# Kernel optimization log

Measured on AMD Instinct MI355X. Metric: run time of the kernel, lower is better.

## Reference

```python
import jax, jax.numpy as jnp
import numpy as np

GROUP = 128  # quantization group size along the input dimension


def dequant(q, scales, zeros):
    # q: [out, in] int4 codes stored as int32 in [0,16)
    # scales, zeros: [out, in//GROUP] per-group affine params
    out_dim, in_dim = q.shape
    g = in_dim // GROUP
    w = (q.astype(jnp.float32).reshape(out_dim, g, GROUP) - zeros[:, :, None]) * scales[:, :, None]
    return w.reshape(out_dim, in_dim)


def setup_inputs() -> dict:
    key = jax.random.key(0)
    ks = jax.random.split(key, 10)
    H, I = 4096, 11008
    B, S = 64, 1
    inp = {
        "x": jax.random.normal(ks[0], (B, S, H), dtype=jnp.float32),
        "gate_qweight": jax.random.randint(ks[1], (I, H), 0, 16, dtype=jnp.int32),
        "gate_scales": jax.random.uniform(ks[2], (I, H // GROUP), dtype=jnp.float32) * 0.02,
        "gate_zeros": jax.random.uniform(ks[3], (I, H // GROUP), dtype=jnp.float32) * 16.0,
        "up_qweight": jax.random.randint(ks[4], (I, H), 0, 16, dtype=jnp.int32),
        "up_scales": jax.random.uniform(ks[5], (I, H // GROUP), dtype=jnp.float32) * 0.02,
        "up_zeros": jax.random.uniform(ks[6], (I, H // GROUP), dtype=jnp.float32) * 16.0,
        "down_qweight": jax.random.randint(ks[7], (H, I), 0, 16, dtype=jnp.int32),
        "down_scales": jax.random.uniform(ks[8], (H, I // GROUP), dtype=jnp.float32) * 0.02,
        "down_zeros": jax.random.uniform(ks[9], (H, I // GROUP), dtype=jnp.float32) * 16.0,
    }
    return inp


def reference(x, gate_qweight, gate_scales, gate_zeros,
              up_qweight, up_scales, up_zeros,
              down_qweight, down_scales, down_zeros):
    Wg = dequant(gate_qweight, gate_scales, gate_zeros)   # [I, H]
    Wu = dequant(up_qweight, up_scales, up_zeros)         # [I, H]
    Wd = dequant(down_qweight, down_scales, down_zeros)   # [H, I]
    gate = jnp.einsum('bsh,ih->bsi', x, Wg)
    up = jnp.einsum('bsh,ih->bsi', x, Wu)
    h = jax.nn.silu(gate) * up                             # SwiGLU
    return jnp.einsum('bsi,hi->bsh', h, Wd)
```

## Files before the change

kernel.cpp:

```cpp
#include <hip/hip_runtime.h>
#include <hip/hip_bf16.h>
#include <stdint.h>

#define H_DIM 4096
#define I_DIM 11008
#define NGH   32
#define NGI   86
#define HP    (H_DIM/8)
#define IP    (I_DIM/8)
#define NWV   5636096

typedef __attribute__((ext_vector_type(8))) short short8;
typedef __attribute__((ext_vector_type(4))) short s16x4;
typedef __attribute__((ext_vector_type(4))) float f32x4;
typedef __attribute__((ext_vector_type(4))) int   i32x4;

static __device__ __forceinline__ short f2bf(float f) {
  union { __hip_bfloat16 b; short s; } u;
  u.b = __float2bfloat16(f);
  return u.s;
}

__global__ void xcvt_kernel(const float* __restrict__ x, short* __restrict__ xb) {
  int i = (blockIdx.x * 256 + threadIdx.x) * 4;
  f32x4 v = *(const f32x4*)(x + i);
  s16x4 o;
  o[0] = f2bf(v[0]); o[1] = f2bf(v[1]); o[2] = f2bf(v[2]); o[3] = f2bf(v[3]);
  *(s16x4*)(xb + i) = o;
}

__global__ __launch_bounds__(256) void pack3_kernel(
    const int* __restrict__ gq, const int* __restrict__ uq, const int* __restrict__ dq,
    int* __restrict__ dst) {
  const int m = blockIdx.x / 22016;
  const int* src = (m == 0) ? gq : (m == 1) ? uq : dq;
  const size_t o = (size_t)(blockIdx.x - m * 22016) * 256 + threadIdx.x;
  const int* s = src + o * 8;
  i32x4 a = *(const i32x4*)s;
  i32x4 b = *(const i32x4*)(s + 4);
  int p = (a[0] & 15)         | ((a[1] & 15) << 4)  | ((a[2] & 15) << 8)  | ((a[3] & 15) << 12)
        | ((b[0] & 15) << 16) | ((b[1] & 15) << 20) | ((b[2] & 15) << 24) | ((b[3] & 15) << 28);
  dst[(size_t)m * NWV + o] = p;
}

__global__ __launch_bounds__(512, 4) void phase1p_kernel(
    const short* __restrict__ xb,
    const int* __restrict__ gp, const float* __restrict__ gsc, const float* __restrict__ gze,
    const int* __restrict__ up, const float* __restrict__ usc, const float* __restrict__ uze,
    short* __restrict__ hb)
{
  __shared__ float red[8][4][4][64];
  const int n0   = blockIdx.x * 16;
  const int w    = threadIdx.x >> 6;
  const int l    = threadIdx.x & 63;
  const int col  = l & 15;
  const int krow = l >> 4;
  const int i    = n0 + col;

  const int*   gpr = gp + (size_t)i * HP;
  const int*   upr = up + (size_t)i * HP;

  float sgv[4], zgv[4], suv[4], zuv[4];
#pragma unroll
  for (int g = 0; g < 4; ++g) {
    const int gg = w * 4 + g;
    sgv[g] = gsc[(size_t)i * NGH + gg];
    zgv[g] = gze[(size_t)i * NGH + gg] * sgv[g];
    suv[g] = usc[(size_t)i * NGH + gg];
    zuv[g] = uze[(size_t)i * NGH + gg] * suv[g];
  }

  f32x4 accG[4], accU[4];
#pragma unroll
  for (int c = 0; c < 4; ++c)
#pragma unroll
    for (int r = 0; r < 4; ++r) { accG[c][r] = 0.f; accU[c][r] = 0.f; }

  const int wb = w * 64;
  const int ks0 = w * 512 + krow * 8;

  int qgA = gpr[wb + krow], quA = upr[wb + krow];
  int qgB, quB;
  short8 aA[4], aB[4];
#pragma unroll
  for (int c = 0; c < 4; ++c)
    aA[c] = *(const short8*)(xb + (size_t)(c * 16 + col) * H_DIM + ks0);

#pragma unroll
  for (int u = 0; u < 8; ++u) {
    const int t1 = 2 * u + 1;
    const int t2 = (2 * u + 2) & 15;
    const int g  = u >> 1;
    qgB = gpr[wb + 4 * t1 + krow];
    quB = upr[wb + 4 * t1 + krow];
#pragma unroll
    for (int c = 0; c < 4; ++c)
      aB[c] = *(const short8*)(xb + (size_t)(c * 16 + col) * H_DIM + ks0 + t1 * 32);
    {
      short8 bg, bu;
#pragma unroll
      for (int j = 0; j < 8; ++j) {
        bg[j] = f2bf((float)((qgA >> (4 * j)) & 15) * sgv[g] - zgv[g]);
        bu[j] = f2bf((float)((quA >> (4 * j)) & 15) * suv[g] - zuv[g]);
      }
#pragma unroll
      for (int c = 0; c < 4; ++c) {
        accG[c] = __builtin_amdgcn_mfma_f32_16x16x32_bf16(aA[c], bg, accG[c], 0, 0, 0);
        accU[c] = __builtin_amdgcn_mfma_f32_16x16x32_bf16(aA[c], bu, accU[c], 0, 0, 0);
      }
    }
    qgA = gpr[wb + 4 * t2 + krow];
    quA = upr[wb + 4 * t2 + krow];
#pragma unroll
    for (int c = 0; c < 4; ++c)
      aA[c] = *(const short8*)(xb + (size_t)(c * 16 + col) * H_DIM + ks0 + t2 * 32);
    {
      short8 bg, bu;
#pragma unroll
      for (int j = 0; j < 8; ++j) {
        bg[j] = f2bf((float)((qgB >> (4 * j)) & 15) * sgv[g] - zgv[g]);
        bu[j] = f2bf((float)((quB >> (4 * j)) & 15) * suv[g] - zuv[g]);
      }
#pragma unroll
      for (int c = 0; c < 4; ++c) {
        accG[c] = __builtin_amdgcn_mfma_f32_16x16x32_bf16(aB[c], bg, accG[c], 0, 0, 0);
        accU[c] = __builtin_amdgcn_mfma_f32_16x16x32_bf16(aB[c], bu, accU[c], 0, 0, 0);
      }
    }
  }

  const int c2 = threadIdx.x >> 7;
  const int rh = (threadIdx.x >> 6) & 1;
  const int ll = threadIdx.x & 63;

#pragma unroll
  for (int c = 0; c < 4; ++c)
#pragma unroll
    for (int r = 0; r < 4; ++r)
      red[w][c][r][l] = accG[c][r];
  __syncthreads();
  float gsum[2];
#pragma unroll
  for (int rr = 0; rr < 2; ++rr) {
    const int r = rh * 2 + rr;
    float s = 0.f;
#pragma unroll
    for (int ww = 0; ww < 8; ++ww) s += red[ww][c2][r][ll];
    gsum[rr] = s;
  }
  __syncthreads();

#pragma unroll
  for (int c = 0; c < 4; ++c)
#pragma unroll
    for (int r = 0; r < 4; ++r)
      red[w][c][r][l] = accU[c][r];
  __syncthreads();
#pragma unroll
  for (int rr = 0; rr < 2; ++rr) {
    const int r = rh * 2 + rr;
    float us = 0.f;
#pragma unroll
    for (int ww = 0; ww < 8; ++ww) us += red[ww][c2][r][ll];
    const float gv = gsum[rr];
    const float hv = gv / (1.f + __expf(-gv)) * us;
    const int m  = c2 * 16 + (ll >> 4) * 4 + r;
    const int ii = n0 + (ll & 15);
    hb[(size_t)m * I_DIM + ii] = f2bf(hv);
  }
}

__global__ __launch_bounds__(512, 4) void phase2p_kernel(
    const short* __restrict__ hb,
    const int* __restrict__ dp, const float* __restrict__ dsc, const float* __restrict__ dze,
    float* __restrict__ part)
{
  __shared__ float red[8][4][4][64];
  const int tile  = blockIdx.x & 255;
  const int split = blockIdx.x >> 8;
  const int n0   = tile * 16;
  const int w    = threadIdx.x >> 6;
  const int l    = threadIdx.x & 63;
  const int col  = l & 15;
  const int krow = l >> 4;
  const int n    = n0 + col;

  const int* dpr = dp + (size_t)n * IP;

  f32x4 acc[4];
#pragma unroll
  for (int c = 0; c < 4; ++c)
#pragma unroll
    for (int r = 0; r < 4; ++r) acc[c][r] = 0.f;

  const int cnt    = (w < 6) ? 11 : 10;
  const int sstart = (w < 6) ? w * 11 : 66 + (w - 6) * 10;
  const int kbase  = split * 2752 + sstart * 32;
  const int wbase  = split * 344 + sstart * 4;

  const int g0 = kbase >> 7;
  float s0 = dsc[(size_t)n * NGI + g0];
  float s1 = dsc[(size_t)n * NGI + min(g0 + 1, NGI - 1)];
  float s2 = dsc[(size_t)n * NGI + min(g0 + 2, NGI - 1)];
  float s3 = dsc[(size_t)n * NGI + min(g0 + 3, NGI - 1)];
  float z0 = dze[(size_t)n * NGI + g0] * s0;
  float z1 = dze[(size_t)n * NGI + min(g0 + 1, NGI - 1)] * s1;
  float z2 = dze[(size_t)n * NGI + min(g0 + 2, NGI - 1)] * s2;
  float z3 = dze[(size_t)n * NGI + min(g0 + 3, NGI - 1)] * s3;

  int qdA = dpr[wbase + krow], qdB;
  short8 aA[4], aB[4];
#pragma unroll
  for (int c = 0; c < 4; ++c)
    aA[c] = *(const short8*)(hb + (size_t)(c * 16 + col) * I_DIM + kbase + krow * 8);

  const int nh = cnt >> 1;
#pragma unroll 1
  for (int u = 0; u < nh; ++u) {
    const int t0 = 2 * u, t1 = 2 * u + 1;
    const int t2 = (t1 + 1 < cnt) ? (t1 + 1) : 0;
    qdB = dpr[wbase + 4 * t1 + krow];
#pragma unroll
    for (int c = 0; c < 4; ++c)
      aB[c] = *(const short8*)(hb + (size_t)(c * 16 + col) * I_DIM + kbase + t1 * 32 + krow * 8);
    {
      const int gi = ((kbase + t0 * 32) >> 7) - g0;
      const float sv = gi == 0 ? s0 : gi == 1 ? s1 : gi == 2 ? s2 : s3;
      const float zv = gi == 0 ? z0 : gi == 1 ? z1 : gi == 2 ? z2 : z3;
      short8 b;
#pragma unroll
      for (int j = 0; j < 8; ++j)
        b[j] = f2bf((float)((qdA >> (4 * j)) & 15) * sv - zv);
#pragma unroll
      for (int c = 0; c < 4; ++c)
        acc[c] = __builtin_amdgcn_mfma_f32_16x16x32_bf16(aA[c], b, acc[c], 0, 0, 0);
    }
    qdA = dpr[wbase + 4 * t2 + krow];
#pragma unroll
    for (int c = 0; c < 4; ++c)
      aA[c] = *(const short8*)(hb + (size_t)(c * 16 + col) * I_DIM + kbase + t2 * 32 + krow * 8);
    {
      const int gi = ((kbase + t1 * 32) >> 7) - g0;
      const float sv = gi == 0 ? s0 : gi == 1 ? s1 : gi == 2 ? s2 : s3;
      const float zv = gi == 0 ? z0 : gi == 1 ? z1 : gi == 2 ? z2 : z3;
      short8 b;
#pragma unroll
      for (int j = 0; j < 8; ++j)
        b[j] = f2bf((float)((qdB >> (4 * j)) & 15) * sv - zv);
#pragma unroll
      for (int c = 0; c < 4; ++c)
        acc[c] = __builtin_amdgcn_mfma_f32_16x16x32_bf16(aB[c], b, acc[c], 0, 0, 0);
    }
  }
  if (cnt & 1) {
    const int t0 = cnt - 1;
    const int gi = ((kbase + t0 * 32) >> 7) - g0;
    const float sv = gi == 0 ? s0 : gi == 1 ? s1 : gi == 2 ? s2 : s3;
    const float zv = gi == 0 ? z0 : gi == 1 ? z1 : gi == 2 ? z2 : z3;
    short8 b;
#pragma unroll
    for (int j = 0; j < 8; ++j)
      b[j] = f2bf((float)((qdA >> (4 * j)) & 15) * sv - zv);
#pragma unroll
    for (int c = 0; c < 4; ++c)
      acc[c] = __builtin_amdgcn_mfma_f32_16x16x32_bf16(aA[c], b, acc[c], 0, 0, 0);
  }

#pragma unroll
  for (int c = 0; c < 4; ++c)
#pragma unroll
    for (int r = 0; r < 4; ++r)
      red[w][c][r][l] = acc[c][r];
  __syncthreads();

  if (threadIdx.x < 256) {
    const int c2 = threadIdx.x >> 6;
    const int ll = threadIdx.x & 63;
    float* po = part + (size_t)split * (64 * H_DIM);
#pragma unroll
    for (int r = 0; r < 4; ++r) {
      float s = 0.f;
#pragma unroll
      for (int ww = 0; ww < 8; ++ww) s += red[ww][c2][r][ll];
      const int m  = c2 * 16 + (ll >> 4) * 4 + r;
      const int nn = n0 + (ll & 15);
      po[(size_t)m * H_DIM + nn] = s;
    }
  }
}

__global__ void reduce4_kernel(const float* __restrict__ part, float* __restrict__ out) {
  const int idx = (blockIdx.x * 256 + threadIdx.x) * 4;
  const int S = 64 * H_DIM;
  f32x4 s0 = *(const f32x4*)(part + idx);
  f32x4 s1 = *(const f32x4*)(part + S + idx);
  f32x4 s2 = *(const f32x4*)(part + 2 * S + idx);
  f32x4 s3 = *(const f32x4*)(part + 3 * S + idx);
  f32x4 r = (s0 + s1) + (s2 + s3);
  *(f32x4*)(out + idx) = r;
}

__global__ __launch_bounds__(512, 4) void phase1f_kernel(
    const short* __restrict__ xb,
    const int* __restrict__ gq, const float* __restrict__ gsc, const float* __restrict__ gze,
    const int* __restrict__ uq, const float* __restrict__ usc, const float* __restrict__ uze,
    short* __restrict__ hb)
{
  __shared__ float red[8][4][4][64];
  const int n0   = blockIdx.x * 16;
  const int w    = threadIdx.x >> 6;
  const int l    = threadIdx.x & 63;
  const int col  = l & 15;
  const int krow = l >> 4;
  const int i    = n0 + col;
  const int*   gqr = gq + (size_t)i * H_DIM;
  const int*   uqr = uq + (size_t)i * H_DIM;
  const float* gsr = gsc + (size_t)i * NGH;
  const float* gzr = gze + (size_t)i * NGH;
  const float* usr = usc + (size_t)i * NGH;
  const float* uzr = uze + (size_t)i * NGH;
  f32x4 accG[4], accU[4];
#pragma unroll
  for (int c = 0; c < 4; ++c)
#pragma unroll
    for (int r = 0; r < 4; ++r) { accG[c][r] = 0.f; accU[c][r] = 0.f; }
  const int kw = w * 512;
  int pk = kw + krow * 8;
  i32x4 nq0 = *(const i32x4*)(gqr + pk);
  i32x4 nq1 = *(const i32x4*)(gqr + pk + 4);
  i32x4 np0 = *(const i32x4*)(uqr + pk);
  i32x4 np1 = *(const i32x4*)(uqr + pk + 4);
#pragma unroll 1
  for (int g = 0; g < 4; ++g) {
    const int gg = w * 4 + g;
    const float sg = gsr[gg], zg = gzr[gg] * sg;
    const float su = usr[gg], zu = uzr[gg] * su;
#pragma unroll
    for (int ks = 0; ks < 4; ++ks) {
      i32x4 q0 = nq0, q1 = nq1, p0 = np0, p1 = np1;
      const int klocal = g * 128 + ks * 32;
      {
        const int nk = kw + ((klocal + 32) & 511) + krow * 8;
        nq0 = *(const i32x4*)(gqr + nk);
        nq1 = *(const i32x4*)(gqr + nk + 4);
        np0 = *(const i32x4*)(uqr + nk);
        np1 = *(const i32x4*)(uqr + nk + 4);
      }
      const int koff = kw + klocal + krow * 8;
      short8 a[4];
#pragma unroll
      for (int c = 0; c < 4; ++c)
        a[c] = *(const short8*)(xb + (size_t)(c * 16 + col) * H_DIM + koff);
      short8 bg, bu;
#pragma unroll
      for (int j = 0; j < 4; ++j) {
        bg[j]     = f2bf((float)q0[j] * sg - zg);
        bg[j + 4] = f2bf((float)q1[j] * sg - zg);
        bu[j]     = f2bf((float)p0[j] * su - zu);
        bu[j + 4] = f2bf((float)p1[j] * su - zu);
      }
#pragma unroll
      for (int c = 0; c < 4; ++c) {
        accG[c] = __builtin_amdgcn_mfma_f32_16x16x32_bf16(a[c], bg, accG[c], 0, 0, 0);
        accU[c] = __builtin_amdgcn_mfma_f32_16x16x32_bf16(a[c], bu, accU[c], 0, 0, 0);
      }
    }
  }
  const int c2 = threadIdx.x >> 7;
  const int rh = (threadIdx.x >> 6) & 1;
  const int ll = threadIdx.x & 63;
#pragma unroll
  for (int c = 0; c < 4; ++c)
#pragma unroll
    for (int r = 0; r < 4; ++r)
      red[w][c][r][l] = accG[c][r];
  __syncthreads();
  float gsum[2];
#pragma unroll
  for (int rr = 0; rr < 2; ++rr) {
    const int r = rh * 2 + rr;
    float s = 0.f;
#pragma unroll
    for (int ww = 0; ww < 8; ++ww) s += red[ww][c2][r][ll];
    gsum[rr] = s;
  }
  __syncthreads();
#pragma unroll
  for (int c = 0; c < 4; ++c)
#pragma unroll
    for (int r = 0; r < 4; ++r)
      red[w][c][r][l] = accU[c][r];
  __syncthreads();
#pragma unroll
  for (int rr = 0; rr < 2; ++rr) {
    const int r = rh * 2 + rr;
    float us = 0.f;
#pragma unroll
    for (int ww = 0; ww < 8; ++ww) us += red[ww][c2][r][ll];
    const float gv = gsum[rr];
    const float hv = gv / (1.f + __expf(-gv)) * us;
    const int m  = c2 * 16 + (ll >> 4) * 4 + r;
    const int ii = n0 + (ll & 15);
    hb[(size_t)m * I_DIM + ii] = f2bf(hv);
  }
}

__global__ __launch_bounds__(512, 4) void phase2f_kernel(
    const short* __restrict__ hb,
    const int* __restrict__ dq, const float* __restrict__ dsc, const float* __restrict__ dze,
    float* __restrict__ part)
{
  __shared__ float red[8][4][4][64];
  const int tile  = blockIdx.x & 255;
  const int split = blockIdx.x >> 8;
  const int n0   = tile * 16;
  const int w    = threadIdx.x >> 6;
  const int l    = threadIdx.x & 63;
  const int col  = l & 15;
  const int krow = l >> 4;
  const int n    = n0 + col;
  const int*   dqr = dq + (size_t)n * I_DIM;
  const float* dsr = dsc + (size_t)n * NGI;
  const float* dzr = dze + (size_t)n * NGI;
  f32x4 acc[4];
#pragma unroll
  for (int c = 0; c < 4; ++c)
#pragma unroll
    for (int r = 0; r < 4; ++r) acc[c][r] = 0.f;
  const int cnt    = (w < 6) ? 11 : 10;
  const int sstart = (w < 6) ? w * 11 : 66 + (w - 6) * 10;
  const int kbase  = split * 2752 + sstart * 32;
  int gprev = -1;
  float sv = 0.f, zv = 0.f;
  int pk = kbase + krow * 8;
  i32x4 nq0 = *(const i32x4*)(dqr + pk);
  i32x4 nq1 = *(const i32x4*)(dqr + pk + 4);
#pragma unroll 1
  for (int s = 0; s < cnt; ++s) {
    i32x4 q0 = nq0, q1 = nq1;
    {
      const int ns = (s + 1 < cnt) ? (s + 1) : 0;
      const int nk = kbase + ns * 32 + krow * 8;
      nq0 = *(const i32x4*)(dqr + nk);
      nq1 = *(const i32x4*)(dqr + nk + 4);
    }
    const int k0 = kbase + s * 32;
    const int g  = k0 >> 7;
    if (g != gprev) { sv = dsr[g]; zv = dzr[g] * sv; gprev = g; }
    short8 a[4];
#pragma unroll
    for (int c = 0; c < 4; ++c)
      a[c] = *(const short8*)(hb + (size_t)(c * 16 + col) * I_DIM + k0 + krow * 8);
    short8 b;
#pragma unroll
    for (int j = 0; j < 4; ++j) {
      b[j]     = f2bf((float)q0[j] * sv - zv);
      b[j + 4] = f2bf((float)q1[j] * sv - zv);
    }
#pragma unroll
    for (int c = 0; c < 4; ++c)
      acc[c] = __builtin_amdgcn_mfma_f32_16x16x32_bf16(a[c], b, acc[c], 0, 0, 0);
  }
#pragma unroll
  for (int c = 0; c < 4; ++c)
#pragma unroll
    for (int r = 0; r < 4; ++r)
      red[w][c][r][l] = acc[c][r];
  __syncthreads();
  if (threadIdx.x < 256) {
    const int c2 = threadIdx.x >> 6;
    const int ll = threadIdx.x & 63;
    float* po = part + (size_t)split * (64 * H_DIM);
#pragma unroll
    for (int r = 0; r < 4; ++r) {
      float s = 0.f;
#pragma unroll
      for (int ww = 0; ww < 8; ++ww) s += red[ww][c2][r][ll];
      const int m  = c2 * 16 + (ll >> 4) * 4 + r;
      const int nn = n0 + (ll & 15);
      po[(size_t)m * H_DIM + nn] = s;
    }
  }
}

extern "C" void kernel_launch(void* const* d_in, const int* in_sizes, int n_in,
                              void* d_out, int out_size, void* d_ws, size_t ws_size,
                              hipStream_t stream) {
  const float* x  = (const float*)d_in[0];
  const int*   gq = (const int*)d_in[1];
  const float* gs = (const float*)d_in[2];
  const float* gz = (const float*)d_in[3];
  const int*   uq = (const int*)d_in[4];
  const float* us = (const float*)d_in[5];
  const float* uz = (const float*)d_in[6];
  const int*   dq = (const int*)d_in[7];
  const float* ds = (const float*)d_in[8];
  const float* dz = (const float*)d_in[9];
  float* out = (float*)d_out;

  const size_t XB   = (size_t)64 * H_DIM * 2;
  const size_t HB   = (size_t)64 * I_DIM * 2;
  const size_t PART = (size_t)4 * 64 * H_DIM * 4;
  const size_t PK   = (size_t)NWV * 4;

  short* xb   = (short*)d_ws;
  short* hb   = (short*)((char*)d_ws + XB);
  float* part = (float*)((char*)d_ws + XB + HB);
  int*   pk   = (int*)((char*)d_ws + XB + HB + PART);
  int*   gp   = pk;
  int*   upk  = pk + NWV;
  int*   dpk  = pk + 2 * (size_t)NWV;

  xcvt_kernel<<<(64 * H_DIM) / 1024, 256, 0, stream>>>(x, xb);

  if (ws_size >= XB + HB + PART + 3 * PK) {
    pack3_kernel<<<3 * 22016, 256, 0, stream>>>(gq, uq, dq, pk);
    phase1p_kernel<<<I_DIM / 16, 512, 0, stream>>>(xb, gp, gs, gz, upk, us, uz, hb);
    phase2p_kernel<<<(H_DIM / 16) * 4, 512, 0, stream>>>(hb, dpk, ds, dz, part);
  } else {
    phase1f_kernel<<<I_DIM / 16, 512, 0, stream>>>(xb, gq, gs, gz, uq, us, uz, hb);
    phase2f_kernel<<<(H_DIM / 16) * 4, 512, 0, stream>>>(hb, dq, ds, dz, part);
  }
  reduce4_kernel<<<(64 * H_DIM) / 1024, 256, 0, stream>>>(part, out);
}
```

Baseline: 243.0 us.

## Pack int4 weights into tiled column-interleaved layout for coalesced GEMM loads

The packing kernel now transposes each 16-row tile through shared memory, so the packed words for the 16 output rows sit next to each other for every k-word. In the GEMM kernels, the 16 lanes that share a krow then read consecutive ints instead of rows strided by the full packed row length. This aims to cut uncoalesced weight traffic in both phases, at the cost of a more complex pack kernel that needs shared memory and a barrier. The fallback kernels also drop their software prefetch of the next weight vectors.

Result: faster. 221.2 us (-8.9%).

```diff
diff --git a/kernel.cpp b/kernel.cpp
--- a/kernel.cpp
+++ b/kernel.cpp
@@ -6,8 +6,8 @@
 #define I_DIM 11008
 #define NGH   32
 #define NGI   86
-#define HP    (H_DIM/8)
-#define IP    (I_DIM/8)
+#define KWH   512
+#define KWI   1376
 #define NWV   5636096
 
 typedef __attribute__((ext_vector_type(8))) short short8;
@@ -29,36 +29,58 @@
   *(s16x4*)(xb + i) = o;
 }
 
-__global__ __launch_bounds__(256) void pack3_kernel(
+__global__ __launch_bounds__(256) void packt_kernel(
     const int* __restrict__ gq, const int* __restrict__ uq, const int* __restrict__ dq,
-    int* __restrict__ dst) {
-  const int m = blockIdx.x / 22016;
-  const int* src = (m == 0) ? gq : (m == 1) ? uq : dq;
-  const size_t o = (size_t)(blockIdx.x - m * 22016) * 256 + threadIdx.x;
-  const int* s = src + o * 8;
-  i32x4 a = *(const i32x4*)s;
-  i32x4 b = *(const i32x4*)(s + 4);
-  int p = (a[0] & 15)         | ((a[1] & 15) << 4)  | ((a[2] & 15) << 8)  | ((a[3] & 15) << 12)
-        | ((b[0] & 15) << 16) | ((b[1] & 15) << 20) | ((b[2] & 15) << 24) | ((b[3] & 15) << 28);
-  dst[(size_t)m * NWV + o] = p;
+    int* __restrict__ pkt) {
+  __shared__ unsigned short sb[16][72];
+  int bid = blockIdx.x;
+  const int* src; int RL, KW; size_t obase; int rt, ct;
+  if (bid < 11008) {
+    src = gq; RL = H_DIM; KW = KWH; obase = 0;
+    rt = bid >> 4; ct = bid & 15;
+  } else if (bid < 22016) {
+    src = uq; RL = H_DIM; KW = KWH; obase = (size_t)NWV;
+    bid -= 11008; rt = bid >> 4; ct = bid & 15;
+  } else {
+    src = dq; RL = I_DIM; KW = KWI; obase = 2 * (size_t)NWV;
+    bid -= 22016; rt = bid / 43; ct = bid - rt * 43;
+  }
+  const int t = threadIdx.x;
+  const int rowl = t >> 4, j = t & 15;
+  const int* rp = src + (size_t)(rt * 16 + rowl) * RL + ct * 256;
+#pragma unroll
+  for (int p = 0; p < 4; ++p) {
+    i32x4 v = *(const i32x4*)(rp + p * 64 + j * 4);
+    sb[rowl][p * 16 + j] = (unsigned short)((v[0] & 15) | ((v[1] & 15) << 4)
+                        | ((v[2] & 15) << 8) | ((v[3] & 15) << 12));
+  }
+  __syncthreads();
+  int* dst = pkt + obase + ((size_t)rt * KW + ct * 32) * 16;
+#pragma unroll
+  for (int p = 0; p < 2; ++p) {
+    const int wi = t + p * 256;
+    const int kwl = wi >> 4, ri = wi & 15;
+    dst[wi] = (int)sb[ri][2 * kwl] | ((int)sb[ri][2 * kwl + 1] << 16);
+  }
 }
 
 __global__ __launch_bounds__(512, 4) void phase1p_kernel(
-    const short* __restrict__ xb,
-    const int* __restrict__ gp, const float* __restrict__ gsc, const float* __restrict__ gze,
-    const int* __restrict__ up, const float* __restrict__ usc, const float* __restrict__ uze,
+    const short* __restrict__ xb, const int* __restrict__ pkt,
+    const float* __restrict__ gsc, const float* __restrict__ gze,
+    const float* __restrict__ usc, const float* __restrict__ uze,
     short* __restrict__ hb)
 {
   __shared__ float red[8][4][4][64];
-  const int n0   = blockIdx.x * 16;
+  const int rt   = blockIdx.x;
+  const int n0   = rt * 16;
   const int w    = threadIdx.x >> 6;
   const int l    = threadIdx.x & 63;
   const int col  = l & 15;
   const int krow = l >> 4;
   const int i    = n0 + col;
 
-  const int*   gpr = gp + (size_t)i * HP;
-  const int*   upr = up + (size_t)i * HP;
+  const int* gB = pkt + (size_t)rt * (KWH * 16) + col;
+  const int* uB = pkt + (size_t)NWV + (size_t)rt * (KWH * 16) + col;
 
   float sgv[4], zgv[4], suv[4], zuv[4];
 #pragma unroll
@@ -76,11 +98,11 @@
 #pragma unroll
     for (int r = 0; r < 4; ++r) { accG[c][r] = 0.f; accU[c][r] = 0.f; }
 
-  const int wb = w * 64;
+  const int wb  = w * 64;
   const int ks0 = w * 512 + krow * 8;
 
-  int qgA = gpr[wb + krow], quA = upr[wb + krow];
-  int qgB, quB;
+  int qgA = gB[(wb + krow) * 16], quA = uB[(wb + krow) * 16];
+  int qgB_, quB_;
   short8 aA[4], aB[4];
 #pragma unroll
   for (int c = 0; c < 4; ++c)
@@ -91,8 +113,8 @@
     const int t1 = 2 * u + 1;
     const int t2 = (2 * u + 2) & 15;
     const int g  = u >> 1;
-    qgB = gpr[wb + 4 * t1 + krow];
-    quB = upr[wb + 4 * t1 + krow];
+    qgB_ = gB[(wb + 4 * t1 + krow) * 16];
+    quB_ = uB[(wb + 4 * t1 + krow) * 16];
 #pragma unroll
     for (int c = 0; c < 4; ++c)
       aB[c] = *(const short8*)(xb + (size_t)(c * 16 + col) * H_DIM + ks0 + t1 * 32);
@@ -109,8 +131,8 @@
         accU[c] = __builtin_amdgcn_mfma_f32_16x16x32_bf16(aA[c], bu, accU[c], 0, 0, 0);
       }
     }
-    qgA = gpr[wb + 4 * t2 + krow];
-    quA = upr[wb + 4 * t2 + krow];
+    qgA = gB[(wb + 4 * t2 + krow) * 16];
+    quA = uB[(wb + 4 * t2 + krow) * 16];
 #pragma unroll
     for (int c = 0; c < 4; ++c)
       aA[c] = *(const short8*)(xb + (size_t)(c * 16 + col) * H_DIM + ks0 + t2 * 32);
@@ -118,8 +140,8 @@
       short8 bg, bu;
 #pragma unroll
       for (int j = 0; j < 8; ++j) {
-        bg[j] = f2bf((float)((qgB >> (4 * j)) & 15) * sgv[g] - zgv[g]);
-        bu[j] = f2bf((float)((quB >> (4 * j)) & 15) * suv[g] - zuv[g]);
+        bg[j] = f2bf((float)((qgB_ >> (4 * j)) & 15) * sgv[g] - zgv[g]);
+        bu[j] = f2bf((float)((quB_ >> (4 * j)) & 15) * suv[g] - zuv[g]);
       }
 #pragma unroll
       for (int c = 0; c < 4; ++c) {
@@ -171,8 +193,8 @@
 }
 
 __global__ __launch_bounds__(512, 4) void phase2p_kernel(
-    const short* __restrict__ hb,
-    const int* __restrict__ dp, const float* __restrict__ dsc, const float* __restrict__ dze,
+    const short* __restrict__ hb, const int* __restrict__ dpt,
+    const float* __restrict__ dsc, const float* __restrict__ dze,
     float* __restrict__ part)
 {
   __shared__ float red[8][4][4][64];
@@ -185,7 +207,7 @@
   const int krow = l >> 4;
   const int n    = n0 + col;
 
-  const int* dpr = dp + (size_t)n * IP;
+  const int* dB = dpt + (size_t)tile * (KWI * 16) + col;
 
   f32x4 acc[4];
 #pragma unroll
@@ -208,7 +230,7 @@
   float z2 = dze[(size_t)n * NGI + min(g0 + 2, NGI - 1)] * s2;
   float z3 = dze[(size_t)n * NGI + min(g0 + 3, NGI - 1)] * s3;
 
-  int qdA = dpr[wbase + krow], qdB;
+  int qdA = dB[(wbase + krow) * 16], qdB_;
   short8 aA[4], aB[4];
 #pragma unroll
   for (int c = 0; c < 4; ++c)
@@ -219,7 +241,7 @@
   for (int u = 0; u < nh; ++u) {
     const int t0 = 2 * u, t1 = 2 * u + 1;
     const int t2 = (t1 + 1 < cnt) ? (t1 + 1) : 0;
-    qdB = dpr[wbase + 4 * t1 + krow];
+    qdB_ = dB[(wbase + 4 * t1 + krow) * 16];
 #pragma unroll
     for (int c = 0; c < 4; ++c)
       aB[c] = *(const short8*)(hb + (size_t)(c * 16 + col) * I_DIM + kbase + t1 * 32 + krow * 8);
@@ -235,7 +257,7 @@
       for (int c = 0; c < 4; ++c)
         acc[c] = __builtin_amdgcn_mfma_f32_16x16x32_bf16(aA[c], b, acc[c], 0, 0, 0);
     }
-    qdA = dpr[wbase + 4 * t2 + krow];
+    qdA = dB[(wbase + 4 * t2 + krow) * 16];
 #pragma unroll
     for (int c = 0; c < 4; ++c)
       aA[c] = *(const short8*)(hb + (size_t)(c * 16 + col) * I_DIM + kbase + t2 * 32 + krow * 8);
@@ -246,7 +268,7 @@
       short8 b;
 #pragma unroll
       for (int j = 0; j < 8; ++j)
-        b[j] = f2bf((float)((qdB >> (4 * j)) & 15) * sv - zv);
+        b[j] = f2bf((float)((qdB_ >> (4 * j)) & 15) * sv - zv);
 #pragma unroll
       for (int c = 0; c < 4; ++c)
         acc[c] = __builtin_amdgcn_mfma_f32_16x16x32_bf16(aB[c], b, acc[c], 0, 0, 0);
@@ -325,11 +347,6 @@
 #pragma unroll
     for (int r = 0; r < 4; ++r) { accG[c][r] = 0.f; accU[c][r] = 0.f; }
   const int kw = w * 512;
-  int pk = kw + krow * 8;
-  i32x4 nq0 = *(const i32x4*)(gqr + pk);
-  i32x4 nq1 = *(const i32x4*)(gqr + pk + 4);
-  i32x4 np0 = *(const i32x4*)(uqr + pk);
-  i32x4 np1 = *(const i32x4*)(uqr + pk + 4);
 #pragma unroll 1
   for (int g = 0; g < 4; ++g) {
     const int gg = w * 4 + g;
@@ -337,16 +354,11 @@
     const float su = usr[gg], zu = uzr[gg] * su;
 #pragma unroll
     for (int ks = 0; ks < 4; ++ks) {
-      i32x4 q0 = nq0, q1 = nq1, p0 = np0, p1 = np1;
-      const int klocal = g * 128 + ks * 32;
-      {
-        const int nk = kw + ((klocal + 32) & 511) + krow * 8;
-        nq0 = *(const i32x4*)(gqr + nk);
-        nq1 = *(const i32x4*)(gqr + nk + 4);
-        np0 = *(const i32x4*)(uqr + nk);
-        np1 = *(const i32x4*)(uqr + nk + 4);
-      }
-      const int koff = kw + klocal + krow * 8;
+      const int koff = kw + g * 128 + ks * 32 + krow * 8;
+      i32x4 q0 = *(const i32x4*)(gqr + koff);
+      i32x4 q1 = *(const i32x4*)(gqr + koff + 4);
+      i32x4 p0 = *(const i32x4*)(uqr + koff);
+      i32x4 p1 = *(const i32x4*)(uqr + koff + 4);
       short8 a[4];
 #pragma unroll
       for (int c = 0; c < 4; ++c)
@@ -432,21 +444,13 @@
   const int kbase  = split * 2752 + sstart * 32;
   int gprev = -1;
   float sv = 0.f, zv = 0.f;
-  int pk = kbase + krow * 8;
-  i32x4 nq0 = *(const i32x4*)(dqr + pk);
-  i32x4 nq1 = *(const i32x4*)(dqr + pk + 4);
 #pragma unroll 1
   for (int s = 0; s < cnt; ++s) {
-    i32x4 q0 = nq0, q1 = nq1;
-    {
-      const int ns = (s + 1 < cnt) ? (s + 1) : 0;
-      const int nk = kbase + ns * 32 + krow * 8;
-      nq0 = *(const i32x4*)(dqr + nk);
-      nq1 = *(const i32x4*)(dqr + nk + 4);
-    }
     const int k0 = kbase + s * 32;
     const int g  = k0 >> 7;
     if (g != gprev) { sv = dsr[g]; zv = dzr[g] * sv; gprev = g; }
+    i32x4 q0 = *(const i32x4*)(dqr + k0 + krow * 8);
+    i32x4 q1 = *(const i32x4*)(dqr + k0 + krow * 8 + 4);
     short8 a[4];
 #pragma unroll
     for (int c = 0; c < 4; ++c)
@@ -506,17 +510,14 @@
   short* xb   = (short*)d_ws;
   short* hb   = (short*)((char*)d_ws + XB);
   float* part = (float*)((char*)d_ws + XB + HB);
-  int*   pk   = (int*)((char*)d_ws + XB + HB + PART);
-  int*   gp   = pk;
-  int*   upk  = pk + NWV;
-  int*   dpk  = pk + 2 * (size_t)NWV;
+  int*   pkt  = (int*)((char*)d_ws + XB + HB + PART);
 
   xcvt_kernel<<<(64 * H_DIM) / 1024, 256, 0, stream>>>(x, xb);
 
   if (ws_size >= XB + HB + PART + 3 * PK) {
-    pack3_kernel<<<3 * 22016, 256, 0, stream>>>(gq, uq, dq, pk);
-    phase1p_kernel<<<I_DIM / 16, 512, 0, stream>>>(xb, gp, gs, gz, upk, us, uz, hb);
-    phase2p_kernel<<<(H_DIM / 16) * 4, 512, 0, stream>>>(hb, dpk, ds, dz, part);
+    packt_kernel<<<33024, 256, 0, stream>>>(gq, uq, dq, pkt);
+    phase1p_kernel<<<I_DIM / 16, 512, 0, stream>>>(xb, pkt, gs, gz, us, uz, hb);
+    phase2p_kernel<<<(H_DIM / 16) * 4, 512, 0, stream>>>(hb, pkt + 2 * (size_t)NWV, ds, dz, part);
   } else {
     phase1f_kernel<<<I_DIM / 16, 512, 0, stream>>>(xb, gq, gs, gz, uq, us, uz, hb);
     phase2f_kernel<<<(H_DIM / 16) * 4, 512, 0, stream>>>(hb, dq, ds, dz, part);
```
